# Optimization experiments

Measured on AMD Instinct MI355X. Metric: run time of the kernel, lower is better.

The kernel has to match this reference:

```python
import jax, jax.numpy as jnp
import numpy as np

B, T, E = 2, 2048, 2048
H = 16
DH = E // H  # 128
FFN = 4 * E  # 8192
EPS = 1e-5


def _layernorm(x, g, b):
    mu = jnp.mean(x, axis=-1, keepdims=True)
    var = jnp.mean((x - mu) ** 2, axis=-1, keepdims=True)
    return (x - mu) * jax.lax.rsqrt(var + EPS) * g + b


def setup_inputs() -> dict:
    key = jax.random.key(0)
    ks = jax.random.split(key, 8)
    s = 0.02
    return {
        "x": jax.random.normal(ks[0], (B, T, E), jnp.float32),
        "g1": jnp.ones((E,), jnp.float32),
        "b1": jnp.zeros((E,), jnp.float32),
        "wq": jax.random.normal(ks[1], (E, E), jnp.float32) * s,
        "wk": jax.random.normal(ks[2], (E, E), jnp.float32) * s,
        "wv": jax.random.normal(ks[3], (E, E), jnp.float32) * s,
        "wo": jax.random.normal(ks[4], (E, E), jnp.float32) * s,
        "g2": jnp.ones((E,), jnp.float32),
        "b2": jnp.zeros((E,), jnp.float32),
        "w1": jax.random.normal(ks[5], (E, FFN), jnp.float32) * s,
        "w2": jax.random.normal(ks[6], (E, FFN), jnp.float32) * s,
        "w3": jax.random.normal(ks[7], (FFN, E), jnp.float32) * s,
    }


def reference(x, g1, b1, wq, wk, wv, wo, g2, b2, w1, w2, w3):
    Bx, Tx, Ex = x.shape
    # --- attention block (pre-LN, residual) ---
    h = _layernorm(x, g1, b1)
    q = (h @ wq).reshape(Bx, Tx, H, DH)
    k = (h @ wk).reshape(Bx, Tx, H, DH)
    v = (h @ wv).reshape(Bx, Tx, H, DH)
    scores = jnp.einsum('bqhd,bkhd->bhqk', q, k) / jnp.sqrt(jnp.float32(DH))
    causal = jnp.tril(jnp.ones((Tx, Tx), bool))  # [T,T]
    scores = jnp.where(causal[None, None], scores, -jnp.inf)
    attn = jax.nn.softmax(scores, axis=-1)
    ctx = jnp.einsum('bhqk,bkhd->bqhd', attn, v).reshape(Bx, Tx, H * DH)
    x = x + ctx @ wo
    # --- SwiGLU MLP block (pre-LN, residual) ---
    h = _layernorm(x, g2, b2)
    gated = jax.nn.silu(h @ w1) * (h @ w2)
    return x + gated @ w3
```

## Files before the change

### kernel.cpp

```cpp
#include <hip/hip_runtime.h>


#define T_SEQ 2048
#define E_DIM 2048
#define N_HEAD 16
#define D_HEAD 128
#define FFN_DIM 8192
#define M_ROWS 4096
#define QKS (2 * E_DIM)

typedef unsigned short u16;
typedef short short8 __attribute__((ext_vector_type(8)));
typedef float f32x4 __attribute__((ext_vector_type(4)));

#define DEV __device__ __forceinline__

DEV u16 f2bf(float f) {
  unsigned u = __float_as_uint(f);
  u += 0x7fffu + ((u >> 16) & 1u);
  return (u16)(u >> 16);
}
DEV float bf2f(u16 h) { return __uint_as_float(((unsigned)h) << 16); }

DEV void async16(void* lds, const void* g) {
  __builtin_amdgcn_global_load_lds((const __attribute__((address_space(1))) void*)g,
                                   (__attribute__((address_space(3))) void*)lds, 16, 0, 0);
}

__global__ __launch_bounds__(256) void ln_kernel(const float* __restrict__ x,
                                                 const float* __restrict__ gw,
                                                 const float* __restrict__ bw,
                                                 u16* __restrict__ out) {
  int row = blockIdx.x;
  int t = threadIdx.x;
  const float4* xr = (const float4*)(x + (size_t)row * E_DIM);
  float4 a = xr[t], c = xr[t + 256];
  float s = a.x + a.y + a.z + a.w + c.x + c.y + c.z + c.w;
  float q = a.x * a.x + a.y * a.y + a.z * a.z + a.w * a.w +
            c.x * c.x + c.y * c.y + c.z * c.z + c.w * c.w;
  for (int off = 32; off > 0; off >>= 1) {
    s += __shfl_down(s, off);
    q += __shfl_down(q, off);
  }
  __shared__ float red[8];
  if ((t & 63) == 0) { red[(t >> 6) * 2] = s; red[(t >> 6) * 2 + 1] = q; }
  __syncthreads();
  s = red[0] + red[2] + red[4] + red[6];
  q = red[1] + red[3] + red[5] + red[7];
  float mu = s * (1.f / E_DIM);
  float rs = rsqrtf(q * (1.f / E_DIM) - mu * mu + 1e-5f);
  const float4* g4 = (const float4*)gw;
  const float4* b4 = (const float4*)bw;
  float4 g0 = g4[t], g1v = g4[t + 256], e0 = b4[t], e1 = b4[t + 256];
  ushort4 o0, o1;
  o0.x = f2bf((a.x - mu) * rs * g0.x + e0.x);
  o0.y = f2bf((a.y - mu) * rs * g0.y + e0.y);
  o0.z = f2bf((a.z - mu) * rs * g0.z + e0.z);
  o0.w = f2bf((a.w - mu) * rs * g0.w + e0.w);
  o1.x = f2bf((c.x - mu) * rs * g1v.x + e1.x);
  o1.y = f2bf((c.y - mu) * rs * g1v.y + e1.y);
  o1.z = f2bf((c.z - mu) * rs * g1v.z + e1.z);
  o1.w = f2bf((c.w - mu) * rs * g1v.w + e1.w);
  ((ushort4*)(out + (size_t)row * E_DIM))[t] = o0;
  ((ushort4*)(out + (size_t)row * E_DIM))[t + 256] = o1;
}

__global__ __launch_bounds__(256) void cvt_all_kernel(
    const float* __restrict__ wq, const float* __restrict__ wk,
    const float* __restrict__ wv, const float* __restrict__ wo,
    const float* __restrict__ w1, const float* __restrict__ w2,
    const float* __restrict__ w3, u16* __restrict__ wqkT,
    u16* __restrict__ wvT, u16* __restrict__ woT, u16* __restrict__ w1T,
    u16* __restrict__ w2T, u16* __restrict__ w3T) {
  __shared__ float tile[32][33];
  const int b = blockIdx.x;
  const float* W;
  u16* WT;
  int Kd, Nd, n0, k0;
  if (b < 16384) {
    int widx = b >> 12, t_ = b & 4095;
    Kd = E_DIM; Nd = E_DIM;
    n0 = (t_ & 63) * 32; k0 = (t_ >> 6) * 32;
    W = widx == 0 ? wq : widx == 1 ? wk : widx == 2 ? wv : wo;
    WT = widx == 0 ? wqkT
         : widx == 1 ? (wqkT + (size_t)E_DIM * E_DIM)
         : widx == 2 ? wvT : woT;
  } else if (b < 49152) {
    int i = b - 16384;
    int widx = i >> 14, t_ = i & 16383;
    Kd = E_DIM; Nd = FFN_DIM;
    n0 = (t_ & 255) * 32; k0 = (t_ >> 8) * 32;
    W = widx ? w2 : w1;
    WT = widx ? w2T : w1T;
  } else {
    int t_ = b - 49152;
    Kd = FFN_DIM; Nd = E_DIM;
    n0 = (t_ & 63) * 32; k0 = (t_ >> 6) * 32;
    W = w3; WT = w3T;
  }
  int tx = threadIdx.x, ty = threadIdx.y;
#pragma unroll
  for (int i = 0; i < 4; i++)
    tile[ty + i * 8][tx] = W[(size_t)(k0 + ty + i * 8) * Nd + n0 + tx];
  __syncthreads();
#pragma unroll
  for (int i = 0; i < 4; i++)
    WT[(size_t)(n0 + ty + i * 8) * Kd + k0 + tx] = f2bf(tile[tx][ty + i * 8]);
}

__global__ __launch_bounds__(256) void transpose_v_kernel(const u16* __restrict__ v,
                                                          u16* __restrict__ vt) {
  __shared__ u16 tile[32][33];
  int tx = threadIdx.x, ty = threadIdx.y;
  int b = blockIdx.z;
  int t0 = blockIdx.x * 32, e0 = blockIdx.y * 32;
#pragma unroll
  for (int i = 0; i < 4; i++)
    tile[ty + i * 8][tx] =
        v[(size_t)(b * T_SEQ + t0 + ty + i * 8) * E_DIM + e0 + tx];
  __syncthreads();
#pragma unroll
  for (int i = 0; i < 4; i++)
    vt[((size_t)b * E_DIM + e0 + ty + i * 8) * T_SEQ + t0 + tx] = tile[tx][ty + i * 8];
}

__global__ __launch_bounds__(256) void add3_kernel(float* __restrict__ out,
                                                   const u16* __restrict__ pk) {
  const size_t MN = (size_t)M_ROWS * E_DIM;
  size_t base = ((size_t)blockIdx.x * 256 + threadIdx.x) * 8;
  short8 a = *(const short8*)(pk + base);
  short8 b = *(const short8*)(pk + MN + base);
  float4 o0 = *(float4*)(out + base), o1 = *(float4*)(out + base + 4);
  o0.x += bf2f((u16)a[0]) + bf2f((u16)b[0]);
  o0.y += bf2f((u16)a[1]) + bf2f((u16)b[1]);
  o0.z += bf2f((u16)a[2]) + bf2f((u16)b[2]);
  o0.w += bf2f((u16)a[3]) + bf2f((u16)b[3]);
  o1.x += bf2f((u16)a[4]) + bf2f((u16)b[4]);
  o1.y += bf2f((u16)a[5]) + bf2f((u16)b[5]);
  o1.z += bf2f((u16)a[6]) + bf2f((u16)b[6]);
  o1.w += bf2f((u16)a[7]) + bf2f((u16)b[7]);
  *(float4*)(out + base) = o0;
  *(float4*)(out + base + 4) = o1;
}

template <int MODE, int BM_>
__global__ __launch_bounds__(512, 1) void gemm8p(const u16* __restrict__ A,
                                                 const u16* __restrict__ BT,
                                                 void* __restrict__ Cout,
                                                 const void* __restrict__ Extra,
                                                 int N, int K, int lda, int ldb,
                                                 int CX, int CY) {
  constexpr int MM = BM_ / 64;
  constexpr int AUNIT = BM_ * 32;
  __shared__ u16 Abuf[4 * AUNIT];
  __shared__ u16 Bbuf[4 * 8192];
  const int t = threadIdx.x;
  const int w = t >> 6, l = t & 63, g = l >> 4, lq = l & 15;
  const int wm = w >> 2, wn = w & 3;

  const int bid = (blockIdx.z * gridDim.y + blockIdx.y) * gridDim.x + blockIdx.x;
  const int xcd = bid & 7, slot = bid >> 3;
  const int nchx = gridDim.x / CX;
  const int nchy = gridDim.y / CY;
  const int cpz = nchx * nchy;
  const int kz = xcd / cpz;
  const int cid = xcd % cpz;
  const int bx = (cid % nchx) * CX + (slot % CX);
  const int by = (cid / nchx) * CY + (slot / CX);
  const size_t bm = (size_t)by * BM_, bn = (size_t)bx * 256;
  const size_t koff = (size_t)kz * K;

  const int srcrow = ((l >> 3) << 1) | (l & 1);
  const int csrc = ((((l >> 1) & 3) ^ ((l >> 3) & 3)) << 3);
  const u16* aSrc = A + (bm + w * 16 + srcrow) * (size_t)lda + koff + csrc;
  const u16* bSrc = BT + (bn + w * 16 + srcrow) * (size_t)ldb + koff + csrc;
  const int rdoff = (((lq & 1) + 2 * (g ^ ((lq >> 1) & 3))) << 3);

#define STA8(DB, KS, TILE)                                                    \
  {                                                                           \
    u16* Ad = Abuf + (DB) * (2 * AUNIT) + (KS)*AUNIT + w * 512;               \
    const u16* as_ = aSrc + (size_t)(TILE)*64 + (KS)*32;                      \
    async16(Ad, as_);                                                         \
    if constexpr (BM_ == 256) async16(Ad + 4096, as_ + (size_t)128 * lda);    \
  }
#define STB8(DB, KS, TILE)                                                    \
  {                                                                           \
    u16* Bd = Bbuf + (DB)*16384 + (KS)*8192 + w * 512;                        \
    const u16* bs_ = bSrc + (size_t)(TILE)*64 + (KS)*32;                      \
    async16(Bd, bs_);                                                         \
    async16(Bd + 4096, bs_ + (size_t)128 * ldb);                              \
  }
#define RDA8(DB, KS, MH)                                                      \
  _Pragma("unroll") for (int mm = 0; mm < MM; ++mm)                           \
      af[mm] = *(const short8*)(Abuf + (DB) * (2 * AUNIT) + (KS)*AUNIT +      \
                                (wm * (BM_ / 4) + (MH) * (BM_ / 8) + mm * 8 + \
                                 (lq >> 1)) * 64 + rdoff);
#define RDB8(DB, KS)                                                          \
  _Pragma("unroll") for (int nn = 0; nn < 4; ++nn)                            \
      bf[nn] = *(const short8*)(Bbuf + (DB)*16384 + (KS)*8192 +               \
                                (wn * 32 + nn * 8 + (lq >> 1)) * 64 + rdoff);
#define MM168(MH)                                                             \
  _Pragma("unroll") for (int mm = 0; mm < MM; ++mm)                           \
      _Pragma("unroll") for (int nn = 0; nn < 4; ++nn)                        \
          acc[(MH)*MM + mm][nn] = __builtin_amdgcn_mfma_f32_16x16x32_bf16(    \
              af[mm], bf[nn], acc[(MH)*MM + mm][nn], 0, 0, 0);
#define SYNCA                                                                 \
  __builtin_amdgcn_s_barrier();                                               \
  asm volatile("s_waitcnt lgkmcnt(0)" ::: "memory");                          \
  __builtin_amdgcn_sched_barrier(0);                                          \
  __builtin_amdgcn_s_setprio(1);
#define ENDP __builtin_amdgcn_s_setprio(0);
#define BAR2 __builtin_amdgcn_s_barrier();
#define WAITN                                                                 \
  if constexpr (BM_ == 256) asm volatile("s_waitcnt vmcnt(8)" ::: "memory");  \
  else                      asm volatile("s_waitcnt vmcnt(6)" ::: "memory");
#define WAITH                                                                 \
  if constexpr (BM_ == 256) asm volatile("s_waitcnt vmcnt(4)" ::: "memory");  \
  else                      asm volatile("s_waitcnt vmcnt(3)" ::: "memory");

  const int NT = K >> 6, NI = NT >> 1;
  f32x4 acc[2 * MM][4] = {};
  short8 af[MM > 4 ? MM : 4], bf[4];

  STA8(0, 0, 0); STB8(0, 0, 0);
  STA8(0, 1, 0); STB8(0, 1, 0);
  STA8(1, 0, 1); STB8(1, 0, 1);
  WAITN;
  BAR2;

  for (int j = 0; j < NI; ++j) {
    const int t1 = 2 * j + 1, t2 = 2 * j + 2, t3 = 2 * j + 3;
    const bool s2 = t2 < NT, s3 = t3 < NT, lastI = (j + 1 == NI);
    RDB8(0, 0); RDA8(0, 0, 0);
    STA8(1, 1, t1);
    SYNCA; MM168(0); ENDP; BAR2;
    RDA8(0, 0, 1);
    STB8(1, 1, t1);
    SYNCA; MM168(1); ENDP;
    WAITN;
    BAR2;
    RDB8(0, 1); RDA8(0, 1, 0);
    if (s2) STA8(0, 0, t2);
    SYNCA; MM168(0); ENDP; BAR2;
    RDA8(0, 1, 1);
    if (s2) STB8(0, 0, t2);
    SYNCA; MM168(1); ENDP;
    if (lastI) { WAITH; } else { WAITN; }
    BAR2;
    RDB8(1, 0); RDA8(1, 0, 0);
    if (s2) STA8(0, 1, t2);
    SYNCA; MM168(0); ENDP; BAR2;
    RDA8(1, 0, 1);
    if (s2) STB8(0, 1, t2);
    SYNCA; MM168(1); ENDP;
    if (lastI) { asm volatile("s_waitcnt vmcnt(0)" ::: "memory"); } else { WAITN; }
    BAR2;
    RDB8(1, 1); RDA8(1, 1, 0);
    if (s3) STA8(1, 0, t3);
    SYNCA; MM168(0); ENDP; BAR2;
    RDA8(1, 1, 1);
    if (s3) STB8(1, 0, t3);
    SYNCA; MM168(1); ENDP;
    if (!lastI) { WAITN; }
    BAR2;
  }
#undef STA8
#undef STB8
#undef RDA8
#undef RDB8
#undef MM168
#undef SYNCA
#undef ENDP
#undef BAR2
#undef WAITN
#undef WAITH

  const size_t mn = (size_t)gridDim.y * BM_ * (size_t)N;
#pragma unroll
  for (int m = 0; m < 2 * MM; m++) {
    size_t row = bm + wm * (BM_ / 2) + m * 16 + 4 * g;
#pragma unroll
    for (int n = 0; n < 4; n++) {
      size_t col = bn + wn * 64 + n * 16 + lq;
#pragma unroll
      for (int r = 0; r < 4; r++) {
        size_t idx = (row + r) * (size_t)N + col;
        if constexpr (MODE == 0) {
          ((u16*)Cout)[idx] = f2bf(acc[m][n][r]);
        } else if constexpr (MODE == 1) {
          ((float*)Cout)[idx] = ((const float*)Extra)[idx] + acc[m][n][r];
        } else if constexpr (MODE == 2) {
          float a = bf2f(((const u16*)Extra)[idx]);
          float sil = a / (1.f + exp2f(-1.4426950408889634f * a));
          ((u16*)Cout)[idx] = f2bf(sil * acc[m][n][r]);
        } else {
          ((u16*)Cout)[(size_t)kz * mn + idx] = f2bf(acc[m][n][r]);
        }
      }
    }
  }
}

__global__ __launch_bounds__(512, 1) void gemm_ffn(const u16* __restrict__ A,
                                                   const u16* __restrict__ B1T,
                                                   const u16* __restrict__ B2T,
                                                   u16* __restrict__ Cout,
                                                   int N, int K, int lda, int ldb,
                                                   int CX, int CY) {
  constexpr int AUNIT = 8192;
  __shared__ u16 Abuf[4 * AUNIT];
  __shared__ u16 Bbuf[4 * AUNIT];
  const int t = threadIdx.x;
  const int w = t >> 6, l = t & 63, g = l >> 4, lq = l & 15;
  const int wm = w >> 2, wn = w & 3;

  const int bid = blockIdx.y * gridDim.x + blockIdx.x;
  const int xcd = bid & 7, slot = bid >> 3;
  const int nchx = gridDim.x / CX;
  const int cid = xcd;
  const int bx = (cid % nchx) * CX + (slot % CX);
  const int by = (cid / nchx) * CY + (slot / CX);
  const size_t bm = (size_t)by * 256;
  const size_t c0 = (size_t)bx * 128;

  const int srcrow = ((l >> 3) << 1) | (l & 1);
  const int csrc = ((((l >> 1) & 3) ^ ((l >> 3) & 3)) << 3);
  const u16* aSrc = A + (bm + w * 16 + srcrow) * (size_t)lda + csrc;
  const u16* b1Src = B1T + (c0 + w * 16 + srcrow) * (size_t)ldb + csrc;
  const u16* b2Src = B2T + (c0 + w * 16 + srcrow) * (size_t)ldb + csrc;
  const int rdoff = (((lq & 1) + 2 * (g ^ ((lq >> 1) & 3))) << 3);

#define STA8(DB, KS, TILE)                                                    \
  {                                                                           \
    u16* Ad = Abuf + (DB) * (2 * AUNIT) + (KS)*AUNIT + w * 512;               \
    const u16* as_ = aSrc + (size_t)(TILE)*64 + (KS)*32;                      \
    async16(Ad, as_);                                                         \
    async16(Ad + 4096, as_ + (size_t)128 * lda);                              \
  }
#define STB8(DB, KS, TILE)                                                    \
  {                                                                           \
    u16* Bd = Bbuf + (DB) * (2 * AUNIT) + (KS)*AUNIT + w * 512;               \
    size_t off_ = (size_t)(TILE)*64 + (KS)*32;                                \
    async16(Bd, b1Src + off_);                                                \
    async16(Bd + 4096, b2Src + off_);                                         \
  }
#define RDA8(DB, KS, MH)                                                      \
  _Pragma("unroll") for (int mm = 0; mm < 4; ++mm)                            \
      af[mm] = *(const short8*)(Abuf + (DB) * (2 * AUNIT) + (KS)*AUNIT +      \
                                (wm * 64 + (MH)*32 + mm * 8 + (lq >> 1)) *    \
                                    64 + rdoff);
#define RDB8(DB, KS)                                                          \
  _Pragma("unroll") for (int nn = 0; nn < 4; ++nn)                            \
      bf[nn] = *(const short8*)(Bbuf + (DB) * (2 * AUNIT) + (KS)*AUNIT +      \
                                (wn * 32 + nn * 8 + (lq >> 1)) * 64 + rdoff);
#define MM168(MH)                                                             \
  _Pragma("unroll") for (int mm = 0; mm < 4; ++mm)                            \
      _Pragma("unroll") for (int nn = 0; nn < 4; ++nn)                        \
          acc[(MH)*4 + mm][nn] = __builtin_amdgcn_mfma_f32_16x16x32_bf16(     \
              af[mm], bf[nn], acc[(MH)*4 + mm][nn], 0, 0, 0);
#define SYNCA                                                                 \
  __builtin_amdgcn_s_barrier();                                               \
  asm volatile("s_waitcnt lgkmcnt(0)" ::: "memory");                          \
  __builtin_amdgcn_sched_barrier(0);                                          \
  __builtin_amdgcn_s_setprio(1);
#define ENDP __builtin_amdgcn_s_setprio(0);
#define BAR2 __builtin_amdgcn_s_barrier();
#define WAITN asm volatile("s_waitcnt vmcnt(8)" ::: "memory");
#define WAITH asm volatile("s_waitcnt vmcnt(4)" ::: "memory");

  const int NT = K >> 6, NI = NT >> 1;
  f32x4 acc[8][4] = {};
  short8 af[4], bf[4];

  STA8(0, 0, 0); STB8(0, 0, 0);
  STA8(0, 1, 0); STB8(0, 1, 0);
  STA8(1, 0, 1); STB8(1, 0, 1);
  WAITN;
  BAR2;

  for (int j = 0; j < NI; ++j) {
    const int t1 = 2 * j + 1, t2 = 2 * j + 2, t3 = 2 * j + 3;
    const bool s2 = t2 < NT, s3 = t3 < NT, lastI = (j + 1 == NI);
    RDB8(0, 0); RDA8(0, 0, 0);
    STA8(1, 1, t1);
    SYNCA; MM168(0); ENDP; BAR2;
    RDA8(0, 0, 1);
    STB8(1, 1, t1);
    SYNCA; MM168(1); ENDP;
    WAITN;
    BAR2;
    RDB8(0, 1); RDA8(0, 1, 0);
    if (s2) STA8(0, 0, t2);
    SYNCA; MM168(0); ENDP; BAR2;
    RDA8(0, 1, 1);
    if (s2) STB8(0, 0, t2);
    SYNCA; MM168(1); ENDP;
    if (lastI) { WAITH; } else { WAITN; }
    BAR2;
    RDB8(1, 0); RDA8(1, 0, 0);
    if (s2) STA8(0, 1, t2);
    SYNCA; MM168(0); ENDP; BAR2;
    RDA8(1, 0, 1);
    if (s2) STB8(0, 1, t2);
    SYNCA; MM168(1); ENDP;
    if (lastI) { asm volatile("s_waitcnt vmcnt(0)" ::: "memory"); } else { WAITN; }
    BAR2;
    RDB8(1, 1); RDA8(1, 1, 0);
    if (s3) STA8(1, 0, t3);
    SYNCA; MM168(0); ENDP; BAR2;
    RDA8(1, 1, 1);
    if (s3) STB8(1, 0, t3);
    SYNCA; MM168(1); ENDP;
    if (!lastI) { WAITN; }
    BAR2;
  }
#undef STA8
#undef STB8
#undef RDA8
#undef RDB8
#undef MM168
#undef SYNCA
#undef ENDP
#undef BAR2
#undef WAITN
#undef WAITH

  const int reg = wm * 2 + ((wn >= 2) ? (wn - 2) : wn);
  float* fb = (float*)((reg < 2 ? Abuf : Bbuf) + (reg & 1) * 16384);
  if (wn >= 2) {
#pragma unroll
    for (int m = 0; m < 8; m++)
#pragma unroll
      for (int n = 0; n < 4; n++)
#pragma unroll
        for (int r = 0; r < 4; r++) {
          int lrow = m * 16 + 4 * g + r;
          int pcol = (n * 16 + lq) ^ ((g & 1) << 4);
          fb[lrow * 64 + pcol] = acc[m][n][r];
        }
  }
  __syncthreads();
  if (wn < 2) {
#pragma unroll
    for (int m = 0; m < 8; m++) {
      size_t row = bm + wm * 128 + m * 16 + 4 * g;
#pragma unroll
      for (int n = 0; n < 4; n++) {
        size_t col = c0 + wn * 64 + n * 16 + lq;
#pragma unroll
        for (int r = 0; r < 4; r++) {
          int lrow = m * 16 + 4 * g + r;
          int pcol = (n * 16 + lq) ^ ((g & 1) << 4);
          float u1 = acc[m][n][r];
          float u2 = fb[lrow * 64 + pcol];
          float sil = u1 / (1.f + exp2f(-1.4426950408889634f * u1));
          Cout[(row + r) * (size_t)N + col] = f2bf(sil * u2);
        }
      }
    }
  }
}

__global__ __launch_bounds__(256, 2) void attn_kernel(const u16* __restrict__ QK,
                                                      const u16* __restrict__ VT,
                                                      u16* __restrict__ CTX) {
  __shared__ u16 Ks[64 * 128];
  __shared__ u16 Vs[128 * 64];
  __shared__ u16 P_all[4][32 * 72];
  const int t = threadIdx.x;
  const int w = t >> 6, l = t & 63, g = l >> 4, lq = l & 15;
  u16* P = P_all[w];
  const int qx = (blockIdx.y & 16) ? (15 - blockIdx.x) : blockIdx.x;
  const int q0blk = qx * 128;
  const int q0w = q0blk + w * 32;
  const int bh = blockIdx.y, b = bh >> 4, h = bh & 15;
  const u16* qp = QK + (size_t)b * T_SEQ * QKS + h * D_HEAD;
  const u16* kp = qp + E_DIM;
  const u16* vp = VT + ((size_t)b * E_DIM + h * D_HEAD) * T_SEQ;

  short8 qf[2][4];
#pragma unroll
  for (int rg = 0; rg < 2; rg++)
#pragma unroll
    for (int ks = 0; ks < 4; ks++)
      qf[rg][ks] =
          *(const short8*)(qp + (size_t)(q0w + rg * 16 + lq) * QKS + ks * 32 + g * 8);

  f32x4 acc[2][8] = {};
  float m2[2][4], ls[2][4];
#pragma unroll
  for (int rg = 0; rg < 2; rg++)
#pragma unroll
    for (int r = 0; r < 4; r++) { m2[rg][r] = -1e30f; ls[rg][r] = 0.f; }
  const float sc = 0.08838834764831845f * 1.4426950408889634f;

  const int kRow0 = 16 * w + (l >> 4);
  const int kChunk = l & 15;
  const int vRow0 = 32 * w + (l >> 3);
  const int vChunk = l & 7;

  for (int kv0 = 0; kv0 < q0blk + 128; kv0 += 64) {
#pragma unroll
    for (int j = 0; j < 4; j++) {
      int R = kRow0 + 4 * j;
      async16(Ks + (16 * w + 4 * j) * 128,
              kp + (size_t)(kv0 + R) * QKS + ((kChunk ^ (R & 7)) << 3));
    }
#pragma unroll
    for (int j = 0; j < 4; j++) {
      int D = vRow0 + 8 * j;
      async16(Vs + (32 * w + 8 * j) * 64,
              vp + (size_t)D * T_SEQ + kv0 + ((vChunk ^ (D & 7)) << 3));
    }
    __syncthreads();

#pragma unroll
    for (int rg = 0; rg < 2; rg++) {
      const int rb = q0w + rg * 16;
      if (kv0 > rb + 15) continue;
      f32x4 s[4];
      __builtin_amdgcn_s_setprio(1);
#pragma unroll
      for (int ct = 0; ct < 4; ct++) {
        s[ct] = f32x4{0.f, 0.f, 0.f, 0.f};
#pragma unroll
        for (int ks = 0; ks < 4; ks++) {
          short8 kf = *(const short8*)(Ks + (ct * 16 + lq) * 128 +
                                       (((ks * 4 + g) ^ (lq & 7)) << 3));
          s[ct] = __builtin_amdgcn_mfma_f32_16x16x32_bf16(qf[rg][ks], kf, s[ct], 0, 0, 0);
        }
      }
      __builtin_amdgcn_s_setprio(0);
      float sv[4][4];
#pragma unroll
      for (int ct = 0; ct < 4; ct++)
#pragma unroll
        for (int r = 0; r < 4; r++) sv[ct][r] = s[ct][r] * sc;
      if (kv0 + 64 > rb) {
#pragma unroll
        for (int ct = 0; ct < 4; ct++)
#pragma unroll
          for (int r = 0; r < 4; r++)
            if (kv0 + ct * 16 + lq > rb + 4 * g + r) sv[ct][r] = -1e30f;
      }
      float mx[4];
#pragma unroll
      for (int r = 0; r < 4; r++)
        mx[r] = fmaxf(fmaxf(sv[0][r], sv[1][r]), fmaxf(sv[2][r], sv[3][r]));
#pragma unroll
      for (int off = 1; off < 16; off <<= 1)
#pragma unroll
        for (int r = 0; r < 4; r++) mx[r] = fmaxf(mx[r], __shfl_xor(mx[r], off));
#pragma unroll
      for (int r = 0; r < 4; r++) {
        float mn = fmaxf(m2[rg][r], mx[r]);
        float sca = exp2f(m2[rg][r] - mn);
        m2[rg][r] = mn;
        float sum = 0.f;
#pragma unroll
        for (int ct = 0; ct < 4; ct++) {
          float pv = exp2f(sv[ct][r] - mn);
          sum += pv;
          P[(rg * 16 + 4 * g + r) * 72 + ct * 16 + lq] = f2bf(pv);
        }
        ls[rg][r] = ls[rg][r] * sca + sum;
#pragma unroll
        for (int n = 0; n < 8; n++) acc[rg][n][r] *= sca;
      }
      short8 pa[2];
#pragma unroll
      for (int ks2 = 0; ks2 < 2; ks2++)
        pa[ks2] = *(const short8*)(P + (rg * 16 + lq) * 72 + ks2 * 32 + g * 8);
      __builtin_amdgcn_s_setprio(1);
#pragma unroll
      for (int n = 0; n < 8; n++)
#pragma unroll
        for (int ks2 = 0; ks2 < 2; ks2++) {
          short8 vf = *(const short8*)(Vs + (n * 16 + lq) * 64 +
                                       (((ks2 * 4 + g) ^ (lq & 7)) << 3));
          acc[rg][n] = __builtin_amdgcn_mfma_f32_16x16x32_bf16(pa[ks2], vf, acc[rg][n], 0, 0, 0);
        }
      __builtin_amdgcn_s_setprio(0);
    }
    __syncthreads();
  }

#pragma unroll
  for (int rg = 0; rg < 2; rg++) {
#pragma unroll
    for (int off = 1; off < 16; off <<= 1)
#pragma unroll
      for (int r = 0; r < 4; r++) ls[rg][r] += __shfl_xor(ls[rg][r], off);
  }
  u16* cp = CTX + ((size_t)b * T_SEQ + q0w) * E_DIM + h * D_HEAD;
#pragma unroll
  for (int rg = 0; rg < 2; rg++) {
    float inv[4];
#pragma unroll
    for (int r = 0; r < 4; r++) inv[r] = 1.f / ls[rg][r];
#pragma unroll
    for (int n = 0; n < 8; n++)
#pragma unroll
      for (int r = 0; r < 4; r++)
        cp[(size_t)(rg * 16 + 4 * g + r) * E_DIM + n * 16 + lq] =
            f2bf(acc[rg][n][r] * inv[r]);
  }
}

extern "C" void kernel_launch(void* const* d_in, const int* in_sizes, int n_in,
                              void* d_out, int out_size, void* d_ws, size_t ws_size,
                              hipStream_t stream) {
  (void)in_sizes; (void)n_in; (void)out_size; (void)ws_size;
  const float* x  = (const float*)d_in[0];
  const float* g1 = (const float*)d_in[1];
  const float* b1 = (const float*)d_in[2];
  const float* wq = (const float*)d_in[3];
  const float* wk = (const float*)d_in[4];
  const float* wv = (const float*)d_in[5];
  const float* wo = (const float*)d_in[6];
  const float* g2 = (const float*)d_in[7];
  const float* b2 = (const float*)d_in[8];
  const float* w1 = (const float*)d_in[9];
  const float* w2 = (const float*)d_in[10];
  const float* w3 = (const float*)d_in[11];
  float* out = (float*)d_out;

  const size_t EE = (size_t)E_DIM * E_DIM;
  const size_t EE2 = EE * 2;
  const size_t EF2 = (size_t)E_DIM * FFN_DIM * 2;
  const size_t ME2 = (size_t)M_ROWS * E_DIM * 2;
  char* p = (char*)d_ws;
  u16* wqkT = (u16*)p; p += 2 * EE2;
  u16* wvT = (u16*)p; p += EE2;
  u16* woT = (u16*)p; p += EE2;
  u16* w1T = (u16*)p; p += EF2;
  u16* w2T = (u16*)p; p += EF2;
  u16* w3T = (u16*)p; p += EF2;
  u16* Hb  = (u16*)p; p += ME2;
  u16* QKb = (u16*)p; p += (size_t)M_ROWS * QKS * 2;
  u16* Vb  = (u16*)p; p += ME2;
  u16* VTb = (u16*)p; p += ME2;
  u16* CTXb = (u16*)p; p += ME2;
  u16* U1b = QKb;
  u16* Pk = wqkT;

  dim3 blk32(32, 8);
  cvt_all_kernel<<<65536, blk32, 0, stream>>>(wq, wk, wv, wo, w1, w2, w3,
                                              wqkT, wvT, woT, w1T, w2T, w3T);

  ln_kernel<<<M_ROWS, 256, 0, stream>>>(x, g1, b1, Hb);
  gemm8p<0, 256><<<dim3(QKS / 256, M_ROWS / 256), 512, 0, stream>>>(
      Hb, wqkT, QKb, nullptr, QKS, E_DIM, E_DIM, E_DIM, 4, 8);
  gemm8p<0, 128><<<dim3(E_DIM / 256, M_ROWS / 128), 512, 0, stream>>>(
      Hb, wvT, Vb, nullptr, E_DIM, E_DIM, E_DIM, E_DIM, 4, 8);
  transpose_v_kernel<<<dim3(T_SEQ / 32, E_DIM / 32, 2), blk32, 0, stream>>>(Vb, VTb);
  attn_kernel<<<dim3(T_SEQ / 128, 2 * N_HEAD), 256, 0, stream>>>(QKb, VTb, CTXb);
  gemm8p<1, 128><<<dim3(E_DIM / 256, M_ROWS / 128), 512, 0, stream>>>(
      CTXb, woT, out, x, E_DIM, E_DIM, E_DIM, E_DIM, 4, 8);

  ln_kernel<<<M_ROWS, 256, 0, stream>>>(out, g2, b2, Hb);
  gemm_ffn<<<dim3(FFN_DIM / 128, M_ROWS / 256), 512, 0, stream>>>(
      Hb, w1T, w2T, U1b, FFN_DIM, E_DIM, E_DIM, E_DIM, 16, 8);
  gemm8p<3, 256><<<dim3(E_DIM / 256, M_ROWS / 256, 2), 512, 0, stream>>>(
      U1b, w3T, Pk, nullptr, E_DIM, FFN_DIM / 2, FFN_DIM, FFN_DIM, 4, 8);
  add3_kernel<<<4096, 256, 0, stream>>>(out, Pk);
}
```

Baseline: 847.8 us.

## Compute V transposed directly via swapped GEMM operands with split-K

Replaces the V projection GEMM plus transpose kernel with a GEMM computing V^T (weights as A, activations as B) split over K into two partial buffers, writing per-batch transposed layout, followed by an elementwise add kernel. This removes the separate transpose pass but adds partial-sum traffic and an extra bf16 rounding on the partials. Partial buffers reuse the weight-QK workspace and the ctx buffer.

Result: no change. 838.8 us (-1.1%).

```diff
diff --git a/kernel.cpp b/kernel.cpp
--- a/kernel.cpp
+++ b/kernel.cpp
@@ -108,22 +108,6 @@
     WT[(size_t)(n0 + ty + i * 8) * Kd + k0 + tx] = f2bf(tile[tx][ty + i * 8]);
 }
 
-__global__ __launch_bounds__(256) void transpose_v_kernel(const u16* __restrict__ v,
-                                                          u16* __restrict__ vt) {
-  __shared__ u16 tile[32][33];
-  int tx = threadIdx.x, ty = threadIdx.y;
-  int b = blockIdx.z;
-  int t0 = blockIdx.x * 32, e0 = blockIdx.y * 32;
-#pragma unroll
-  for (int i = 0; i < 4; i++)
-    tile[ty + i * 8][tx] =
-        v[(size_t)(b * T_SEQ + t0 + ty + i * 8) * E_DIM + e0 + tx];
-  __syncthreads();
-#pragma unroll
-  for (int i = 0; i < 4; i++)
-    vt[((size_t)b * E_DIM + e0 + ty + i * 8) * T_SEQ + t0 + tx] = tile[tx][ty + i * 8];
-}
-
 __global__ __launch_bounds__(256) void add3_kernel(float* __restrict__ out,
                                                    const u16* __restrict__ pk) {
   const size_t MN = (size_t)M_ROWS * E_DIM;
@@ -141,6 +125,19 @@
   o1.w += bf2f((u16)a[7]) + bf2f((u16)b[7]);
   *(float4*)(out + base) = o0;
   *(float4*)(out + base + 4) = o1;
+}
+
+__global__ __launch_bounds__(256) void addv_kernel(u16* __restrict__ vt,
+                                                   const u16* __restrict__ pv0,
+                                                   const u16* __restrict__ pv1) {
+  size_t base = ((size_t)blockIdx.x * 256 + threadIdx.x) * 8;
+  short8 a = *(const short8*)(pv0 + base);
+  short8 b = *(const short8*)(pv1 + base);
+  short8 o;
+#pragma unroll
+  for (int i = 0; i < 8; i++)
+    o[i] = (short)f2bf(bf2f((u16)a[i]) + bf2f((u16)b[i]));
+  *(short8*)(vt + base) = o;
 }
 
 template <int MODE, int BM_>
@@ -293,8 +290,12 @@
           float a = bf2f(((const u16*)Extra)[idx]);
           float sil = a / (1.f + exp2f(-1.4426950408889634f * a));
           ((u16*)Cout)[idx] = f2bf(sil * acc[m][n][r]);
+        } else if constexpr (MODE == 3) {
+          ((u16*)Cout)[(size_t)kz * mn + idx] = f2bf(acc[m][n][r]);
         } else {
-          ((u16*)Cout)[(size_t)kz * mn + idx] = f2bf(acc[m][n][r]);
+          size_t bb = col >> 11, tt = col & 2047;
+          u16* dst = kz ? (u16*)Extra : (u16*)Cout;
+          dst[(bb * E_DIM + row + r) * (size_t)T_SEQ + tt] = f2bf(acc[m][n][r]);
         }
       }
     }
@@ -638,10 +639,11 @@
   u16* w3T = (u16*)p; p += EF2;
   u16* Hb  = (u16*)p; p += ME2;
   u16* QKb = (u16*)p; p += (size_t)M_ROWS * QKS * 2;
-  u16* Vb  = (u16*)p; p += ME2;
   u16* VTb = (u16*)p; p += ME2;
   u16* CTXb = (u16*)p; p += ME2;
   u16* U1b = QKb;
+  u16* Pv0 = wqkT;
+  u16* Pv1 = CTXb;
   u16* Pk = wqkT;
 
   dim3 blk32(32, 8);
@@ -651,9 +653,9 @@
   ln_kernel<<<M_ROWS, 256, 0, stream>>>(x, g1, b1, Hb);
   gemm8p<0, 256><<<dim3(QKS / 256, M_ROWS / 256), 512, 0, stream>>>(
       Hb, wqkT, QKb, nullptr, QKS, E_DIM, E_DIM, E_DIM, 4, 8);
-  gemm8p<0, 128><<<dim3(E_DIM / 256, M_ROWS / 128), 512, 0, stream>>>(
-      Hb, wvT, Vb, nullptr, E_DIM, E_DIM, E_DIM, E_DIM, 4, 8);
-  transpose_v_kernel<<<dim3(T_SEQ / 32, E_DIM / 32, 2), blk32, 0, stream>>>(Vb, VTb);
+  gemm8p<4, 256><<<dim3(M_ROWS / 256, E_DIM / 256, 2), 512, 0, stream>>>(
+      wvT, Hb, Pv0, Pv1, M_ROWS, E_DIM / 2, E_DIM, E_DIM, 8, 4);
+  addv_kernel<<<4096, 256, 0, stream>>>(VTb, Pv0, Pv1);
   attn_kernel<<<dim3(T_SEQ / 128, 2 * N_HEAD), 256, 0, stream>>>(QKb, VTb, CTXb);
   gemm8p<1, 128><<<dim3(E_DIM / 256, M_ROWS / 128), 512, 0, stream>>>(
       CTXb, woT, out, x, E_DIM, E_DIM, E_DIM, E_DIM, 4, 8);
```
